# Performance work log

Hardware: AMD Instinct MI355X
Metric: run time of the kernel (lower is better)

Reference implementation:

```python
import jax, jax.numpy as jnp
import numpy as np

B, N, E, C, K, D, L, FC, IN, OUT = 2, 40000, 320000, 128, 64, 2, 4, 128, 3, 1


def _gelu(x):
    return jax.nn.gelu(x, approximate=False)  # torch F.gelu default = exact erf


def _compute_gradient(f, tgt, src, egw):
    # f: [B,C,N]; tgt,src: [B,E] int; egw: [B,E,D] -> returns [B, C*D, N]
    fT = f.transpose(0, 2, 1)  # [B,N,C]
    diff = jnp.take_along_axis(fT, src[..., None], axis=1) - jnp.take_along_axis(fT, tgt[..., None], axis=1)  # [B,E,C]
    msg = (diff[:, :, :, None] * egw[:, :, None, :]).reshape(fT.shape[0], tgt.shape[1], -1)  # [B,E,C*D], c outer / d inner
    g = jnp.zeros((fT.shape[0], fT.shape[1], msg.shape[-1]), f.dtype)
    g = g.at[jnp.arange(fT.shape[0])[:, None], tgt].add(msg)  # scatter_add over target nodes
    return g.transpose(0, 2, 1)


def _spectral(x, wc, ws, w0, bc, bs, b0, wbc, wbs, wb0):
    # x: [B,Cin,N]; wc/ws: [Cin,Cout,K]; w0: [Cin,Cout,1]; bases: [B,N,K] or [B,N,1]
    xc = jnp.einsum('bix,bxk->bik', x, wbc)
    xs = -jnp.einsum('bix,bxk->bik', x, wbs)
    x0 = jnp.einsum('bix,bxk->bik', x, wb0)
    fc = jnp.einsum('bik,iok->bok', xc, wc) - jnp.einsum('bik,iok->bok', xs, ws)
    fs = jnp.einsum('bik,iok->bok', xs, wc) + jnp.einsum('bik,iok->bok', xc, ws)
    f0 = jnp.einsum('bik,iok->bok', x0, w0)
    return (jnp.einsum('bok,bxk->box', f0, b0)
            + 2.0 * jnp.einsum('bok,bxk->box', fc, bc)
            - 2.0 * jnp.einsum('bok,bxk->box', fs, bs))


def _forward(x, node_mask, nodes, node_weights, edge_gradient_weights, modes,
             fc0_w, fc0_b, sp_wc, sp_ws, sp_w0, w_w, w_b, gw_w, gw_b,
             fc1_w, fc1_b, fc2_w, fc2_b, directed_edges):
    temp = jnp.einsum('bxd,kd->bxk', nodes, modes)
    bc = jnp.cos(temp) * node_mask
    bs = jnp.sin(temp) * node_mask
    b0 = node_mask
    wbc, wbs, wb0 = bc * node_weights, bs * node_weights, b0 * node_weights
    h = (x @ fc0_w + fc0_b).transpose(0, 2, 1)  # lift -> [B,C,N]
    tgt = directed_edges[..., 0]
    src = directed_edges[..., 1]
    nl = sp_wc.shape[0]
    for i in range(nl):
        x1 = _spectral(h, sp_wc[i], sp_ws[i], sp_w0[i], bc, bs, b0, wbc, wbs, wb0)
        x2 = jnp.einsum('oc,bcn->bon', w_w[i], h) + w_b[i][None, :, None]  # 1x1 conv
        # x3 is computed but NOT added, exactly matching the source (x = x1 + x2)
        x3 = jnp.einsum('oc,bcn->bon', gw_w[i],
                        jax.nn.soft_sign(_compute_gradient(h, tgt, src, edge_gradient_weights))) + gw_b[i][None, :, None]
        h = x1 + x2
        if i != nl - 1:
            h = _gelu(h)
    h = h.transpose(0, 2, 1)  # [B,N,C]
    h = _gelu(h @ fc1_w + fc1_b)
    return h @ fc2_w + fc2_b  # [B,N,OUT]


def setup_inputs() -> dict:
    key = jax.random.key(0)
    ks = jax.random.split(key, 16)
    scale = 1.0 / float(C * C)
    return {
        'x': jax.random.normal(ks[0], (B, N, IN), jnp.float32),
        'node_mask': jnp.ones((B, N, 1), jnp.float32),
        'nodes': jax.random.uniform(ks[1], (B, N, D), jnp.float32),
        'node_weights': jax.random.uniform(ks[2], (B, N, 1), jnp.float32) * (1.0 / N),
        'directed_edges': jax.random.randint(ks[3], (B, E, 2), 0, N, dtype=jnp.int32),
        'edge_gradient_weights': jax.random.normal(ks[4], (B, E, D), jnp.float32) * 0.1,
        'modes': jax.random.normal(ks[5], (K, D), jnp.float32) * 4.0,
        'fc0_w': jax.random.normal(ks[6], (IN, C), jnp.float32) * float(1.0 / np.sqrt(IN)),
        'fc0_b': jnp.zeros((C,), jnp.float32),
        'sp_wc': jax.random.uniform(ks[7], (L, C, C, K), jnp.float32) * scale,
        'sp_ws': jax.random.uniform(ks[8], (L, C, C, K), jnp.float32) * scale,
        'sp_w0': jax.random.uniform(ks[9], (L, C, C, 1), jnp.float32) * scale,
        'w_w': jax.random.normal(ks[10], (L, C, C), jnp.float32) * float(1.0 / np.sqrt(C)),
        'w_b': jnp.zeros((L, C), jnp.float32),
        'gw_w': jax.random.normal(ks[11], (L, C, D * C), jnp.float32) * float(1.0 / np.sqrt(D * C)),
        'gw_b': jnp.zeros((L, C), jnp.float32),
        'fc1_w': jax.random.normal(ks[12], (C, FC), jnp.float32) * float(1.0 / np.sqrt(C)),
        'fc1_b': jnp.zeros((FC,), jnp.float32),
        'fc2_w': jax.random.normal(ks[13], (FC, OUT), jnp.float32) * float(1.0 / np.sqrt(FC)),
        'fc2_b': jnp.zeros((OUT,), jnp.float32),
    }


def reference(x, node_mask, nodes, node_weights, directed_edges, edge_gradient_weights, modes,
              fc0_w, fc0_b, sp_wc, sp_ws, sp_w0, w_w, w_b, gw_w, gw_b,
              fc1_w, fc1_b, fc2_w, fc2_b):
    return _forward(x, node_mask, nodes, node_weights, edge_gradient_weights, modes,
                    fc0_w, fc0_b, sp_wc, sp_ws, sp_w0, w_w, w_b, gw_w, gw_b,
                    fc1_w, fc1_b, fc2_w, fc2_b, directed_edges)
```

## Files before the change

### kernel.cpp

```cpp
#include <hip/hip_runtime.h>
#include <math.h>

#define NN 40000
#define NP 40064
#define CC 128
#define KK 64
#define BATCH 2
#define NLAYER 4
#define FSPLITS 128
#define MODES 144
#define KTOT 256
#define NCH 626
#define NVCH 625

typedef __attribute__((ext_vector_type(8))) short bf16x8;
typedef __attribute__((ext_vector_type(4))) float f32x4;
typedef __attribute__((ext_vector_type(4))) unsigned short u16x4;
typedef __attribute__((ext_vector_type(8))) unsigned short u16x8;

__device__ __forceinline__ float gelu_exact(float x) {
    return 0.5f * x * (1.0f + erff(x * 0.70710678118654752f));
}
__device__ __forceinline__ unsigned short f2bf(float x) {
    unsigned int u = __float_as_uint(x);
    u += 0x7FFFu + ((u >> 16) & 1u);
    return (unsigned short)(u >> 16);
}
__device__ __forceinline__ float bf2f(unsigned short v) {
    return __uint_as_float(((unsigned int)v) << 16);
}
__device__ __forceinline__ void bar_lgkm() {
    asm volatile("s_waitcnt lgkmcnt(0)" ::: "memory");
    __builtin_amdgcn_s_barrier();
}

__global__ void fc1t_kernel(const float* __restrict__ fc1, unsigned short* __restrict__ fc1t) {
    int idx = blockIdx.x * 256 + threadIdx.x;
    int f = idx >> 7, c = idx & 127;
    fc1t[f * 128 + c] = f2bf(fc1[c * 128 + f]);
}

__global__ __launch_bounds__(512) void lift_fused(const float* __restrict__ x,
        const float* __restrict__ w, const float* __restrict__ bvec,
        const float* __restrict__ nodes, const float* __restrict__ mask,
        const float* __restrict__ wts, const float* __restrict__ modes,
        unsigned short* __restrict__ Binv, float* __restrict__ maskp,
        float* __restrict__ warr, unsigned short* __restrict__ pxcs) {
    int s = blockIdx.x, b = blockIdx.y;
    int t = threadIdx.x, wv = t >> 6, l = t & 63, lo = l & 15, hi = l >> 4;
    __shared__ __align__(16) char lds[53504];
    char* Ts   = lds;
    char* Ts2  = lds + 16384;
    char* Wt   = lds + 32768;
    float* xl  = (float*)(lds + 51200);
    float* ndl = (float*)(lds + 51968);
    float* wl  = (float*)(lds + 52480);
    float* ml  = (float*)(lds + 52736);
    float* sm  = (float*)(lds + 52992);
    int c = t & 127, ng = t >> 7;
    float w0 = w[c], w1 = w[CC + c], w2 = w[2 * CC + c], bv = bvec[c];
    f32x4 accF[9];
    #pragma unroll
    for (int mt = 0; mt < 9; ++mt) accF[mt] = (f32x4){0.f, 0.f, 0.f, 0.f};
    if (t < 128) sm[t] = modes[t];
    if (t < 480) *(unsigned int*)(Wt + 129 * 128 + t * 4) = 0u;

    auto fetch = [&](int chunk) -> float {
        if (chunk >= NVCH) return 0.f;
        long base = (long)b * NN + chunk * 64;
        if (t < 192) return x[base * 3 + t];
        if (t < 320) return nodes[base * 2 + (t - 192)];
        if (t < 384) return wts[base + (t - 320)];
        if (t < 448) return mask[base + (t - 384)];
        return 0.f;
    };
    float pf = fetch(s);

    for (int chunk = s; chunk < NCH; chunk += FSPLITS) {
        int nbase = chunk * 64;
        bar_lgkm();
        {
            if (t < 192)      xl[t] = pf;
            else if (t < 320) ndl[t - 192] = pf;
            else if (t < 384) wl[t - 320] = pf;
            else if (t < 448) ml[t - 384] = pf;
        }
        int nc = chunk + FSPLITS;
        if (nc < NCH) pf = fetch(nc);
        bar_lgkm();
        {
            int n_ = t & 63, g = t >> 6;
            float nx = ndl[n_ * 2], ny = ndl[n_ * 2 + 1];
            float m = ml[n_];
            u16x8 cosr, sinr;
            #pragma unroll
            for (int j = 0; j < 8; ++j) {
                int k = g * 8 + j;
                float tv = nx * sm[2 * k] + ny * sm[2 * k + 1];
                float sv, cv;
                __sincosf(tv, &sv, &cv);
                unsigned short cb = f2bf(cv * m), sb = f2bf(sv * m);
                cosr[j] = cb; sinr[j] = sb;
                *(unsigned short*)(Wt + ((k * 128 + n_ * 2) ^ ((k & 7) << 4))) = cb;
                *(unsigned short*)(Wt + (((64 + k) * 128 + n_ * 2) ^ (((64 + k) & 7) << 4))) = sb;
            }
            char* brow = (char*)Binv + ((long)b * NP + nbase + n_) * 512 + g * 16;
            *(u16x8*)brow = cosr;
            *(u16x8*)(brow + 128) = sinr;
            if (t < 64) {
                *(unsigned short*)(Wt + 128 * 128 + n_ * 2) = f2bf(m);
                maskp[(long)b * NP + nbase + n_] = m;
                warr[(long)b * NP + nbase + n_] = wl[n_];
            }
        }
        {
            u16x8 hv0, hv1;
            #pragma unroll
            for (int j = 0; j < 16; ++j) {
                int n = ng * 16 + j;
                float h = bv + xl[n * 3] * w0 + xl[n * 3 + 1] * w1 + xl[n * 3 + 2] * w2;
                unsigned short hb = f2bf(h);
                unsigned short hwb = f2bf(h * wl[n]);
                if (j < 8) hv0[j] = hwb; else hv1[j - 8] = hwb;
                *(unsigned short*)(Ts + (((n << 8) + c * 2) ^ ((n & 7) << 4))) = hb;
            }
            int base2 = c * 128 + ng * 32;
            *(u16x8*)(Ts2 + (base2 ^ ((c & 7) << 4))) = hv0;
            *(u16x8*)(Ts2 + ((base2 + 16) ^ ((c & 7) << 4))) = hv1;
        }
        bar_lgkm();
        char* Bdst = (char*)Binv + ((long)b * NP + nbase) * 512 + 256;
        #pragma unroll
        for (int pass = 0; pass < 2; ++pass) {
            int n = pass * 32 + (t >> 4), seg = t & 15;
            uint4 v = *(const uint4*)(Ts + (((n << 8) + (seg << 4)) ^ ((n & 7) << 4)));
            *(uint4*)(Bdst + (long)n * 512 + seg * 16) = v;
        }
        int ct = wv * 16;
        #pragma unroll
        for (int ks2 = 0; ks2 < 2; ++ks2) {
            int ar = ct + lo;
            bf16x8 a = *(const bf16x8*)(Ts2 + ((ar * 128 + ks2 * 64 + hi * 16) ^ ((ar & 7) << 4)));
            #pragma unroll
            for (int mt = 0; mt < 9; ++mt) {
                int mrow = mt * 16 + lo;
                bf16x8 bb = *(const bf16x8*)(Wt + ((mrow * 128 + ks2 * 64 + hi * 16) ^ ((mrow & 7) << 4)));
                accF[mt] = __builtin_amdgcn_mfma_f32_16x16x32_bf16(a, bb, accF[mt], 0, 0, 0);
            }
        }
    }
    unsigned short* pb = pxcs + ((long)s * BATCH + b) * CC * MODES;
    #pragma unroll
    for (int mt = 0; mt < 9; ++mt)
        #pragma unroll
        for (int r = 0; r < 4; ++r)
            pb[(long)(wv * 16 + hi * 4 + r) * MODES + mt * 16 + lo] = f2bf(accF[mt][r]);
}

__global__ __launch_bounds__(256) void reduce_kernel(const unsigned short* __restrict__ pxcs,
        float* __restrict__ xc, float* __restrict__ xs, float* __restrict__ x0) {
    int gid = blockIdx.x * 256 + threadIdx.x;
    int idx = gid >> 3, sg = gid & 7;
    float a = 0.f;
    #pragma unroll
    for (int j = 0; j < 16; ++j)
        a += bf2f(pxcs[(long)(sg * 16 + j) * (BATCH * CC * MODES) + idx]);
    a += __shfl_xor(a, 1); a += __shfl_xor(a, 2); a += __shfl_xor(a, 4);
    if (sg == 0) {
        int m = idx % MODES, bc_ = idx / MODES;
        if (m < 64)        xc[bc_ * KK + m] = a;
        else if (m < 128)  xs[bc_ * KK + m - 64] = a;
        else if (m == 128) x0[bc_] = a;
    }
}

__global__ __launch_bounds__(1024) void mix_kernel(const float* __restrict__ xc,
        const float* __restrict__ xs, const float* __restrict__ x0,
        const float* __restrict__ wc, const float* __restrict__ wsp,
        const float* __restrict__ w0, const float* __restrict__ ww,
        const float* __restrict__ wbias, unsigned short* __restrict__ A,
        float* __restrict__ f0a, float* __restrict__ wba, int layer) {
    int o = blockIdx.x, b = blockIdx.y;
    int k = threadIdx.x & 63, ig = threadIdx.x >> 6;
    const float* wcl = wc  + (long)layer * CC * CC * KK;
    const float* wsl = wsp + (long)layer * CC * CC * KK;
    float fc = 0.f, fs = 0.f;
    #pragma unroll
    for (int j = 0; j < 8; ++j) {
        int i = ig * 8 + j;
        float xci = xc[(b * CC + i) * KK + k];
        float xsi = xs[(b * CC + i) * KK + k];
        float wcv = wcl[((long)i * CC + o) * KK + k];
        float wsv = wsl[((long)i * CC + o) * KK + k];
        fc += xci * wcv + xsi * wsv;
        fs += xci * wsv - xsi * wcv;
    }
    __shared__ float rc[16][64], rs[16][64];
    rc[ig][k] = fc; rs[ig][k] = fs;
    __syncthreads();
    unsigned short* Ar = A + ((long)b * CC + o) * KTOT;
    if (ig == 0) {
        fc = 0.f; fs = 0.f;
        #pragma unroll
        for (int j = 0; j < 16; ++j) { fc += rc[j][k]; fs += rs[j][k]; }
        Ar[k]      = f2bf(2.f * fc);
        Ar[64 + k] = f2bf(-2.f * fs);
    } else if (ig == 1) {
        const float* wwl = ww + ((long)layer * CC + o) * CC;
        Ar[128 + k] = f2bf(wwl[k]);
        Ar[192 + k] = f2bf(wwl[64 + k]);
    } else if (ig == 2) {
        const float* w0l = w0 + (long)layer * CC * CC;
        float p = x0[b * CC + k] * w0l[(long)k * CC + o]
                + x0[b * CC + 64 + k] * w0l[(long)(64 + k) * CC + o];
        #pragma unroll
        for (int off = 32; off > 0; off >>= 1) p += __shfl_down(p, off, 64);
        if (k == 0) { f0a[b * CC + o] = p; wba[b * CC + o] = wbias[layer * CC + o]; }
    }
}

template <int DO_FWD, int DOGELU>
__global__ __launch_bounds__(512) void fused_inv(const unsigned short* __restrict__ Amat,
        unsigned short* Binv, const float* __restrict__ f0a, const float* __restrict__ wba,
        const float* __restrict__ maskp, const float* __restrict__ warr,
        unsigned short* __restrict__ pxcs) {
    int s = blockIdx.x, b = blockIdx.y;
    int t = threadIdx.x, wv = t >> 6, l = t & 63, lo = l & 15, hi = l >> 4;
    int wo = wv & 3, wn = wv >> 2;
    int obase = wo * 32, nwin = wn * 32;
    __shared__ __align__(16) char lds[51712];
    char* Btile = lds;
    char* Ts    = lds;
    char* Ts2   = lds + 16384;
    char* Wt    = lds + 32768;
    float* ml   = (float*)(lds + 51200);
    float* wl   = (float*)(lds + 51456);
    const unsigned short* Ab = Amat + (long)b * CC * KTOT;
    bf16x8 af[2][8];
    f32x4 f0v[2], wbv[2];
    #pragma unroll
    for (int fr = 0; fr < 2; ++fr) {
        const unsigned short* arow = Ab + (long)(obase + fr * 16 + lo) * KTOT + hi * 8;
        #pragma unroll
        for (int ks = 0; ks < 8; ++ks) af[fr][ks] = *(const bf16x8*)(arow + ks * 32);
        int o0f = obase + fr * 16 + hi * 4;
        f0v[fr] = *(const f32x4*)(f0a + b * CC + o0f);
        wbv[fr] = *(const f32x4*)(wba + b * CC + o0f);
    }
    int swz = (lo & 7) << 4;
    f32x4 accF[9];
    #pragma unroll
    for (int mt = 0; mt < 9; ++mt) accF[mt] = (f32x4){0.f, 0.f, 0.f, 0.f};
    const char* Bbase = (const char*)Binv + (long)b * NP * 512;
    if (DO_FWD && t < 480) *(unsigned int*)(Wt + 129 * 128 + t * 4) = 0u;

    uint4 pB0 = {}, pB1 = {}, pB2 = {}, pB3 = {};
    float pmv = 0.f, pwv = 0.f;
    {
        const char* Bsrc = Bbase + (long)s * 64 * 512;
        pB0 = *(const uint4*)(Bsrc + 0 * 8192 + t * 16);
        pB1 = *(const uint4*)(Bsrc + 1 * 8192 + t * 16);
        pB2 = *(const uint4*)(Bsrc + 2 * 8192 + t * 16);
        pB3 = *(const uint4*)(Bsrc + 3 * 8192 + t * 16);
        if (t < 64) { pmv = maskp[(long)b * NP + s * 64 + t]; pwv = warr[(long)b * NP + s * 64 + t]; }
    }

    for (int chunk = s; chunk < NCH; chunk += FSPLITS) {
        int nbase = chunk * 64;
        bar_lgkm();
        {
            int o = 0 * 8192 + t * 16; *(uint4*)(Btile + (o ^ (((o >> 9) & 7) << 4))) = pB0;
            o = 1 * 8192 + t * 16;     *(uint4*)(Btile + (o ^ (((o >> 9) & 7) << 4))) = pB1;
            o = 2 * 8192 + t * 16;     *(uint4*)(Btile + (o ^ (((o >> 9) & 7) << 4))) = pB2;
            o = 3 * 8192 + t * 16;     *(uint4*)(Btile + (o ^ (((o >> 9) & 7) << 4))) = pB3;
            if (t < 64) { ml[t] = pmv; wl[t] = pwv; }
        }
        int nc = chunk + FSPLITS;
        if (nc < NCH) {
            const char* Bsrc = Bbase + (long)nc * 64 * 512;
            pB0 = *(const uint4*)(Bsrc + 0 * 8192 + t * 16);
            pB1 = *(const uint4*)(Bsrc + 1 * 8192 + t * 16);
            pB2 = *(const uint4*)(Bsrc + 2 * 8192 + t * 16);
            pB3 = *(const uint4*)(Bsrc + 3 * 8192 + t * 16);
            if (t < 64) { pmv = maskp[(long)b * NP + nc * 64 + t]; pwv = warr[(long)b * NP + nc * 64 + t]; }
        }
        bar_lgkm();
        if (DO_FWD) {
            int g = t >> 6, n_ = t & 63;
            int rkey = (n_ & 7) << 4;
            int raddr = n_ * 512 + g * 32;
            u16x8 r0 = *(const u16x8*)(Btile + (raddr ^ rkey));
            u16x8 r1 = *(const u16x8*)(Btile + ((raddr + 16) ^ rkey));
            #pragma unroll
            for (int i = 0; i < 8; ++i) {
                int mr = g * 16 + i;
                *(unsigned short*)(Wt + ((mr * 128 + n_ * 2) ^ ((mr & 7) << 4))) = r0[i];
            }
            #pragma unroll
            for (int i = 0; i < 8; ++i) {
                int mr = g * 16 + 8 + i;
                *(unsigned short*)(Wt + ((mr * 128 + n_ * 2) ^ ((mr & 7) << 4))) = r1[i];
            }
            if (t < 64) *(unsigned short*)(Wt + 128 * 128 + t * 2) = f2bf(ml[t]);
        }
        f32x4 acc[2][2];
        #pragma unroll
        for (int fr = 0; fr < 2; ++fr)
            #pragma unroll
            for (int fn = 0; fn < 2; ++fn) acc[fr][fn] = (f32x4){0.f, 0.f, 0.f, 0.f};
        #pragma unroll
        for (int ks = 0; ks < 8; ++ks) {
            #pragma unroll
            for (int fn = 0; fn < 2; ++fn) {
                int boff = ((nwin + fn * 16 + lo) << 9) + (ks << 6) + (hi << 4);
                bf16x8 bb = *(const bf16x8*)(Btile + (boff ^ swz));
                acc[0][fn] = __builtin_amdgcn_mfma_f32_16x16x32_bf16(af[0][ks], bb, acc[0][fn], 0, 0, 0);
                acc[1][fn] = __builtin_amdgcn_mfma_f32_16x16x32_bf16(af[1][ks], bb, acc[1][fn], 0, 0, 0);
            }
        }
        bar_lgkm();
        #pragma unroll
        for (int fr = 0; fr < 2; ++fr) {
            int o0 = obase + fr * 16 + hi * 4;
            #pragma unroll
            for (int fn = 0; fn < 2; ++fn) {
                int n = nwin + fn * 16 + lo;
                float mv = ml[n];
                u16x4 pk;
                #pragma unroll
                for (int r = 0; r < 4; ++r) {
                    float v = acc[fr][fn][r] + f0v[fr][r] * mv + wbv[fr][r];
                    if (DOGELU) v = gelu_exact(v);
                    pk[r] = f2bf(v);
                    if (DO_FWD)
                        *(unsigned short*)(Ts2 + (((o0 + r) * 128 + n * 2) ^ (((o0 + r) & 7) << 4))) = f2bf(v * wl[n]);
                }
                *(u16x4*)(Ts + (((n << 8) + (o0 << 1)) ^ ((n & 7) << 4))) = pk;
            }
        }
        bar_lgkm();
        char* Bdst = (char*)Binv + ((long)b * NP + nbase) * 512 + 256;
        #pragma unroll
        for (int pass = 0; pass < 2; ++pass) {
            int n = pass * 32 + (t >> 4), seg = t & 15;
            uint4 v = *(const uint4*)(Ts + (((n << 8) + (seg << 4)) ^ ((n & 7) << 4)));
            *(uint4*)(Bdst + (long)n * 512 + seg * 16) = v;
        }
        if (DO_FWD) {
            int ct = wv * 16;
            #pragma unroll
            for (int ks2 = 0; ks2 < 2; ++ks2) {
                int ar = ct + lo;
                bf16x8 a = *(const bf16x8*)(Ts2 + ((ar * 128 + ks2 * 64 + hi * 16) ^ ((ar & 7) << 4)));
                #pragma unroll
                for (int mt = 0; mt < 9; ++mt) {
                    int mrow = mt * 16 + lo;
                    bf16x8 bb = *(const bf16x8*)(Wt + ((mrow * 128 + ks2 * 64 + hi * 16) ^ ((mrow & 7) << 4)));
                    accF[mt] = __builtin_amdgcn_mfma_f32_16x16x32_bf16(a, bb, accF[mt], 0, 0, 0);
                }
            }
        }
    }
    if (DO_FWD) {
        unsigned short* pb = pxcs + ((long)s * BATCH + b) * CC * MODES;
        #pragma unroll
        for (int mt = 0; mt < 9; ++mt)
            #pragma unroll
            for (int r = 0; r < 4; ++r)
                pb[(long)(wv * 16 + hi * 4 + r) * MODES + mt * 16 + lo] = f2bf(accF[mt][r]);
    }
}

__global__ __launch_bounds__(256) void head_mfma(const unsigned short* __restrict__ Binv,
        const unsigned short* __restrict__ fc1t, const float* __restrict__ b1,
        const float* __restrict__ fc2, const float* __restrict__ b2, float* __restrict__ out) {
    int t = threadIdx.x, wv = t >> 6, l = t & 63, lo = l & 15, hi = l >> 4;
    int b = blockIdx.y;
    int nb = (blockIdx.x * 4 + wv) * 16;
    const unsigned short* Arow = Binv + ((long)b * NP + nb + lo) * KTOT + 128 + hi * 8;
    f32x4 acc[8];
    #pragma unroll
    for (int ft = 0; ft < 8; ++ft) acc[ft] = (f32x4){0.f, 0.f, 0.f, 0.f};
    #pragma unroll
    for (int ks = 0; ks < 4; ++ks) {
        bf16x8 a = *(const bf16x8*)(Arow + ks * 32);
        #pragma unroll
        for (int ft = 0; ft < 8; ++ft) {
            bf16x8 bv = *(const bf16x8*)(fc1t + (ft * 16 + lo) * 128 + ks * 32 + hi * 8);
            acc[ft] = __builtin_amdgcn_mfma_f32_16x16x32_bf16(a, bv, acc[ft], 0, 0, 0);
        }
    }
    float s[4] = {0.f, 0.f, 0.f, 0.f};
    #pragma unroll
    for (int ft = 0; ft < 8; ++ft) {
        int f = ft * 16 + lo;
        float b1f = b1[f], f2f = fc2[f];
        #pragma unroll
        for (int r = 0; r < 4; ++r) s[r] += gelu_exact(acc[ft][r] + b1f) * f2f;
    }
    float b2v = b2[0];
    #pragma unroll
    for (int r = 0; r < 4; ++r) {
        float v = s[r];
        v += __shfl_xor(v, 1); v += __shfl_xor(v, 2);
        v += __shfl_xor(v, 4); v += __shfl_xor(v, 8);
        if (lo == 0) out[(long)b * NN + nb + hi * 4 + r] = v + b2v;
    }
}

extern "C" void kernel_launch(void* const* d_in, const int* in_sizes, int n_in,
                              void* d_out, int out_size, void* d_ws, size_t ws_size,
                              hipStream_t stream) {
    const float* x     = (const float*)d_in[0];
    const float* mask  = (const float*)d_in[1];
    const float* nodes = (const float*)d_in[2];
    const float* wts   = (const float*)d_in[3];
    const float* modes = (const float*)d_in[6];
    const float* fc0w  = (const float*)d_in[7];
    const float* fc0b  = (const float*)d_in[8];
    const float* spwc  = (const float*)d_in[9];
    const float* spws  = (const float*)d_in[10];
    const float* spw0  = (const float*)d_in[11];
    const float* ww    = (const float*)d_in[12];
    const float* wb    = (const float*)d_in[13];
    const float* fc1w  = (const float*)d_in[16];
    const float* fc1b  = (const float*)d_in[17];
    const float* fc2w  = (const float*)d_in[18];
    const float* fc2b  = (const float*)d_in[19];

    char* p = (char*)d_ws;
    auto alloc = [&](size_t bytes) { char* r = p; p += (bytes + 255) & ~255UL; return r; };
    unsigned short* Binv = (unsigned short*)alloc((size_t)BATCH * NP * KTOT * 2);
    unsigned short* Amat = (unsigned short*)alloc((size_t)BATCH * CC * KTOT * 2);
    unsigned short* fc1t = (unsigned short*)alloc((size_t)CC * 128 * 2);
    unsigned short* pxcs = (unsigned short*)alloc((size_t)FSPLITS * BATCH * CC * MODES * 2);
    float* xcb  = (float*)alloc((size_t)BATCH * CC * KK * 4);
    float* xsb  = (float*)alloc((size_t)BATCH * CC * KK * 4);
    float* x0b  = (float*)alloc((size_t)BATCH * CC * 4);
    float* f0a  = (float*)alloc((size_t)BATCH * CC * 4);
    float* wba  = (float*)alloc((size_t)BATCH * CC * 4);
    float* maskp = (float*)alloc((size_t)BATCH * NP * 4);
    float* warr  = (float*)alloc((size_t)BATCH * NP * 4);

    fc1t_kernel<<<64, 256, 0, stream>>>(fc1w, fc1t);
    lift_fused<<<dim3(FSPLITS, BATCH), 512, 0, stream>>>(x, fc0w, fc0b, nodes, mask, wts,
                                                         modes, Binv, maskp, warr, pxcs);

    for (int l = 0; l < NLAYER; ++l) {
        reduce_kernel<<<(8 * BATCH * CC * MODES) / 256, 256, 0, stream>>>(pxcs, xcb, xsb, x0b);
        mix_kernel<<<dim3(CC, BATCH), 1024, 0, stream>>>(xcb, xsb, x0b, spwc, spws, spw0,
                                                         ww, wb, Amat, f0a, wba, l);
        if (l < NLAYER - 1)
            fused_inv<1, 1><<<dim3(FSPLITS, BATCH), 512, 0, stream>>>(
                Amat, Binv, f0a, wba, maskp, warr, pxcs);
        else
            fused_inv<0, 0><<<dim3(FSPLITS, BATCH), 512, 0, stream>>>(
                Amat, Binv, f0a, wba, maskp, warr, pxcs);
    }
    head_mfma<<<dim3(NN / 64, BATCH), 256, 0, stream>>>(Binv, fc1t, fc1b, fc2w, fc2b, (float*)d_out);
}
```

Baseline: 197.9 us.

## Double-buffer the B tile in LDS and drop per-chunk barriers

```diff
diff --git a/kernel.cpp b/kernel.cpp
--- a/kernel.cpp
+++ b/kernel.cpp
@@ -228,13 +228,10 @@
     int t = threadIdx.x, wv = t >> 6, l = t & 63, lo = l & 15, hi = l >> 4;
     int wo = wv & 3, wn = wv >> 2;
     int obase = wo * 32, nwin = wn * 32;
-    __shared__ __align__(16) char lds[51712];
-    char* Btile = lds;
-    char* Ts    = lds;
-    char* Ts2   = lds + 16384;
-    char* Wt    = lds + 32768;
-    float* ml   = (float*)(lds + 51200);
-    float* wl   = (float*)(lds + 51456);
+    __shared__ __align__(16) char lds[117760];
+    char* Ts  = lds + 65536;
+    char* Ts2 = lds + 81920;
+    char* Wt  = lds + 98304;
     const unsigned short* Ab = Amat + (long)b * CC * KTOT;
     bf16x8 af[2][8];
     f32x4 f0v[2], wbv[2];
@@ -256,41 +253,51 @@
 
     uint4 pB0 = {}, pB1 = {}, pB2 = {}, pB3 = {};
     float pmv = 0.f, pwv = 0.f;
-    {
-        const char* Bsrc = Bbase + (long)s * 64 * 512;
+    auto issue = [&](int chunk) {
+        const char* Bsrc = Bbase + (long)chunk * 64 * 512;
         pB0 = *(const uint4*)(Bsrc + 0 * 8192 + t * 16);
         pB1 = *(const uint4*)(Bsrc + 1 * 8192 + t * 16);
         pB2 = *(const uint4*)(Bsrc + 2 * 8192 + t * 16);
         pB3 = *(const uint4*)(Bsrc + 3 * 8192 + t * 16);
-        if (t < 64) { pmv = maskp[(long)b * NP + s * 64 + t]; pwv = warr[(long)b * NP + s * 64 + t]; }
-    }
-
-    for (int chunk = s; chunk < NCH; chunk += FSPLITS) {
+        if (t < 64) {
+            pmv = maskp[(long)b * NP + chunk * 64 + t];
+            pwv = warr[(long)b * NP + chunk * 64 + t];
+        }
+    };
+    auto commit = [&](char* Bq, float* mq) {
+        int o = 0 * 8192 + t * 16; *(uint4*)(Bq + (o ^ (((o >> 9) & 7) << 4))) = pB0;
+        o = 1 * 8192 + t * 16;     *(uint4*)(Bq + (o ^ (((o >> 9) & 7) << 4))) = pB1;
+        o = 2 * 8192 + t * 16;     *(uint4*)(Bq + (o ^ (((o >> 9) & 7) << 4))) = pB2;
+        o = 3 * 8192 + t * 16;     *(uint4*)(Bq + (o ^ (((o >> 9) & 7) << 4))) = pB3;
+        if (t < 64) { mq[t] = pmv; mq[64 + t] = pwv; }
+    };
+
+    {
+        issue(s);
+        commit(lds, (float*)(lds + 116736));
+        if (s + FSPLITS < NCH) issue(s + FSPLITS);
+    }
+    bar_lgkm();
+
+    int iter = 0;
+    for (int chunk = s; chunk < NCH; chunk += FSPLITS, ++iter) {
+        int P = iter & 1;
+        char* BtP = lds + P * 32768;
+        char* BtQ = lds + (P ^ 1) * 32768;
+        float* mqP = (float*)(lds + 116736 + P * 512);
+        float* mqQ = (float*)(lds + 116736 + (P ^ 1) * 512);
         int nbase = chunk * 64;
-        bar_lgkm();
-        {
-            int o = 0 * 8192 + t * 16; *(uint4*)(Btile + (o ^ (((o >> 9) & 7) << 4))) = pB0;
-            o = 1 * 8192 + t * 16;     *(uint4*)(Btile + (o ^ (((o >> 9) & 7) << 4))) = pB1;
-            o = 2 * 8192 + t * 16;     *(uint4*)(Btile + (o ^ (((o >> 9) & 7) << 4))) = pB2;
-            o = 3 * 8192 + t * 16;     *(uint4*)(Btile + (o ^ (((o >> 9) & 7) << 4))) = pB3;
-            if (t < 64) { ml[t] = pmv; wl[t] = pwv; }
-        }
         int nc = chunk + FSPLITS;
         if (nc < NCH) {
-            const char* Bsrc = Bbase + (long)nc * 64 * 512;
-            pB0 = *(const uint4*)(Bsrc + 0 * 8192 + t * 16);
-            pB1 = *(const uint4*)(Bsrc + 1 * 8192 + t * 16);
-            pB2 = *(const uint4*)(Bsrc + 2 * 8192 + t * 16);
-            pB3 = *(const uint4*)(Bsrc + 3 * 8192 + t * 16);
-            if (t < 64) { pmv = maskp[(long)b * NP + nc * 64 + t]; pwv = warr[(long)b * NP + nc * 64 + t]; }
-        }
-        bar_lgkm();
+            commit(BtQ, mqQ);
+            if (nc + FSPLITS < NCH) issue(nc + FSPLITS);
+        }
         if (DO_FWD) {
             int g = t >> 6, n_ = t & 63;
             int rkey = (n_ & 7) << 4;
             int raddr = n_ * 512 + g * 32;
-            u16x8 r0 = *(const u16x8*)(Btile + (raddr ^ rkey));
-            u16x8 r1 = *(const u16x8*)(Btile + ((raddr + 16) ^ rkey));
+            u16x8 r0 = *(const u16x8*)(BtP + (raddr ^ rkey));
+            u16x8 r1 = *(const u16x8*)(BtP + ((raddr + 16) ^ rkey));
             #pragma unroll
             for (int i = 0; i < 8; ++i) {
                 int mr = g * 16 + i;
@@ -301,7 +308,7 @@
                 int mr = g * 16 + 8 + i;
                 *(unsigned short*)(Wt + ((mr * 128 + n_ * 2) ^ ((mr & 7) << 4))) = r1[i];
             }
-            if (t < 64) *(unsigned short*)(Wt + 128 * 128 + t * 2) = f2bf(ml[t]);
+            if (t < 64) *(unsigned short*)(Wt + 128 * 128 + t * 2) = f2bf(mqP[t]);
         }
         f32x4 acc[2][2];
         #pragma unroll
@@ -313,19 +320,18 @@
             #pragma unroll
             for (int fn = 0; fn < 2; ++fn) {
                 int boff = ((nwin + fn * 16 + lo) << 9) + (ks << 6) + (hi << 4);
-                bf16x8 bb = *(const bf16x8*)(Btile + (boff ^ swz));
+                bf16x8 bb = *(const bf16x8*)(BtP + (boff ^ swz));
                 acc[0][fn] = __builtin_amdgcn_mfma_f32_16x16x32_bf16(af[0][ks], bb, acc[0][fn], 0, 0, 0);
                 acc[1][fn] = __builtin_amdgcn_mfma_f32_16x16x32_bf16(af[1][ks], bb, acc[1][fn], 0, 0, 0);
             }
         }
-        bar_lgkm();
         #pragma unroll
         for (int fr = 0; fr < 2; ++fr) {
             int o0 = obase + fr * 16 + hi * 4;
             #pragma unroll
             for (int fn = 0; fn < 2; ++fn) {
                 int n = nwin + fn * 16 + lo;
-                float mv = ml[n];
+                float mv = mqP[n];
                 u16x4 pk;
                 #pragma unroll
                 for (int r = 0; r < 4; ++r) {
@@ -333,7 +339,7 @@
                     if (DOGELU) v = gelu_exact(v);
                     pk[r] = f2bf(v);
                     if (DO_FWD)
-                        *(unsigned short*)(Ts2 + (((o0 + r) * 128 + n * 2) ^ (((o0 + r) & 7) << 4))) = f2bf(v * wl[n]);
+                        *(unsigned short*)(Ts2 + (((o0 + r) * 128 + n * 2) ^ (((o0 + r) & 7) << 4))) = f2bf(v * mqP[64 + n]);
                 }
                 *(u16x4*)(Ts + (((n << 8) + (o0 << 1)) ^ ((n & 7) << 4))) = pk;
             }
@@ -360,6 +366,7 @@
                 }
             }
         }
+        bar_lgkm();
     }
     if (DO_FWD) {
         unsigned short* pb = pxcs + ((long)s * BATCH + b) * CC * MODES;
```

Result: slower. 209.7 us (+6.0%).
